# Optimization experiments

Measured on AMD Instinct MI355X. Metric: run time of the kernel, lower is better.

Reference implementation:

```python
import jax, jax.numpy as jnp
import numpy as np

B, L, D, H = 2, 2048, 1024, 16
DK = D // H


def setup_inputs() -> dict:
    key = jax.random.key(0)
    ks = jax.random.split(key, 12)
    s = 1.0 / np.sqrt(D)
    inp = {
        "query": jax.random.normal(ks[0], (B, L, D), jnp.float32),
        "key_": jax.random.normal(ks[1], (B, L, D), jnp.float32),
        "value": jax.random.normal(ks[2], (B, L, D), jnp.float32),
        # causal boolean mask, broadcast over heads: (B, 1, L_q, L_k)
        "mask": jnp.broadcast_to(jnp.tril(jnp.ones((L, L), jnp.bool_)), (B, 1, L, L)),
        "w_q": jax.random.uniform(ks[3], (D, D), jnp.float32, -s, s),
        "b_q": jax.random.uniform(ks[4], (D,), jnp.float32, -s, s),
        "w_k": jax.random.uniform(ks[5], (D, D), jnp.float32, -s, s),
        "b_k": jax.random.uniform(ks[6], (D,), jnp.float32, -s, s),
        "w_v": jax.random.uniform(ks[7], (D, D), jnp.float32, -s, s),
        "b_v": jax.random.uniform(ks[8], (D,), jnp.float32, -s, s),
        "w_o": jax.random.uniform(ks[9], (D, D), jnp.float32, -s, s),
        "b_o": jax.random.uniform(ks[10], (D,), jnp.float32, -s, s),
    }
    return inp


def reference(query, key_, value, mask, w_q, b_q, w_k, b_k, w_v, b_v, w_o, b_o):
    # torch nn.Linear: y = x @ W.T + b, weight shape (out, in)
    Q = query @ w_q.T + b_q
    K = key_ @ w_k.T + b_k
    V = value @ w_v.T + b_v
    # (B, L, H, DK) -> (B, H, L, DK)
    Q = Q.reshape(B, L, H, DK).transpose(0, 2, 1, 3)
    K = K.reshape(B, L, H, DK).transpose(0, 2, 1, 3)
    V = V.reshape(B, L, H, DK).transpose(0, 2, 1, 3)
    scaling = jnp.sqrt(jnp.float32(DK))
    scores = jnp.einsum("bhqd,bhkd->bhqk", Q, K) / scaling  # (B,H,L,L)
    scores = jnp.where(mask, scores, jnp.float32(-1e9))
    attn = jax.nn.softmax(scores, axis=-1)
    out = jnp.einsum("bhqk,bhkd->bhqd", attn, V)  # (B,H,L,DK)
    out = out.transpose(0, 2, 1, 3).reshape(B, L, D)
    return out @ w_o.T + b_o
```

## Files before the change

### kernel.cpp

```cpp
#include <hip/hip_runtime.h>
#include <stdint.h>

#define Bb 2
#define Ll 2048
#define Dd 1024
#define Hh 16
#define DKd 64
#define Mm (Bb*Ll)

typedef __bf16 bf16_t;
typedef __bf16 bf16x8 __attribute__((ext_vector_type(8)));
typedef float f32x4 __attribute__((ext_vector_type(4)));
typedef unsigned u32x2 __attribute__((ext_vector_type(2)));

#define AS1C(p) ((const __attribute__((address_space(1))) void*)(p))
#define AS3(p)  ((__attribute__((address_space(3))) void*)(p))

__device__ __forceinline__ unsigned short bfu(float f){
  return __builtin_bit_cast(unsigned short, (bf16_t)f);
}
__device__ __forceinline__ void wait_vm4(){ asm volatile("s_waitcnt vmcnt(4)" ::: "memory"); }
__device__ __forceinline__ void wait_vm6(){ asm volatile("s_waitcnt vmcnt(6)" ::: "memory"); }
__device__ __forceinline__ void wait_vm0(){ asm volatile("s_waitcnt vmcnt(0)" ::: "memory"); }
__device__ __forceinline__ void bar(){
  __builtin_amdgcn_sched_barrier(0);
  __builtin_amdgcn_s_barrier();
  __builtin_amdgcn_sched_barrier(0);
}

struct Cvt4 { const float* in[4]; ushort4* out[4]; };

__global__ void cvt_multi(Cvt4 a, int n4){
  const int z = blockIdx.y;
  int i = blockIdx.x*256 + threadIdx.x;
  if (i < n4){
    float4 v = ((const float4*)a.in[z])[i];
    ushort4 o; o.x=bfu(v.x); o.y=bfu(v.y); o.z=bfu(v.z); o.w=bfu(v.w);
    a.out[z][i] = o;
  }
}

struct GemmArgs {
  const void*   A[3];
  const bf16_t* W[3];
  const float*  bias[3];
  void*         out[3];
  float         scale[3];
  int           mode[3];
};

#define BKs 64

__global__ __launch_bounds__(256) void gemm128_f32(GemmArgs ga, int M, int N, int K)
{
  const int z = blockIdx.z;
  const float*  __restrict__ A  = (const float*)ga.A[z];
  const bf16_t* __restrict__ Bw = ga.W[z];
  const float*  __restrict__ bias = ga.bias[z];
  void* __restrict__ out = ga.out[z];
  const float scale = ga.scale[z];
  const int mode = ga.mode[z];

  __shared__ float  As[128*BKs];
  __shared__ bf16_t Bs[128*BKs];
  const int tid = threadIdx.x;
  const int lane = tid & 63;
  const int w = tid >> 6;
  const int m0 = blockIdx.x * 128;
  const int n0 = blockIdx.y * 128;
  const int wr = (w >> 1) * 64, wc = (w & 1) * 64;
  const int lrow16 = lane & 15;
  const int kgrp = lane >> 4;

  const int arow4 = lane >> 4;
  const int acb   = (lane & 15) * 16;
  const int brow8 = lane >> 3;
  const int bcb   = (lane & 7) * 16;

  f32x4 acc[4][4] = {};

  for (int k0 = 0; k0 < K; k0 += BKs) {
#pragma unroll
    for (int i = 0; i < 8; i++) {
      int c = i*4 + w;
      int row = c*4 + arow4;
      int sb = acb ^ ((row & 7) << 4);
      __builtin_amdgcn_global_load_lds(AS1C(A + (size_t)(m0+row)*K + k0 + (sb >> 2)),
                                       AS3((char*)As + c*1024), 16, 0, 0);
    }
#pragma unroll
    for (int i = 0; i < 4; i++) {
      int c = i*4 + w;
      int row = c*8 + brow8;
      int sb = bcb ^ ((row & 7) << 4);
      __builtin_amdgcn_global_load_lds(AS1C((const char*)(Bw + (size_t)(n0+row)*K + k0) + sb),
                                       AS3((char*)Bs + c*1024), 16, 0, 0);
    }
    __syncthreads();
#pragma unroll
    for (int ks = 0; ks < 2; ++ks) {
      bf16x8 af[4], bfr[4];
      const int akb = ks*128 + kgrp*32;
      const int bkb = ks*64 + kgrp*16;
#pragma unroll
      for (int m = 0; m < 4; m++) {
        int row = wr + m*16 + lrow16;
        int swz = (row & 7) << 4;
        const char* rb = (const char*)As + row*256;
        float4 lo = *(const float4*)(rb + (akb ^ swz));
        float4 hi = *(const float4*)(rb + ((akb + 16) ^ swz));
        bf16x8 a;
        a[0]=(bf16_t)lo.x; a[1]=(bf16_t)lo.y; a[2]=(bf16_t)lo.z; a[3]=(bf16_t)lo.w;
        a[4]=(bf16_t)hi.x; a[5]=(bf16_t)hi.y; a[6]=(bf16_t)hi.z; a[7]=(bf16_t)hi.w;
        af[m] = a;
      }
#pragma unroll
      for (int n = 0; n < 4; n++) {
        int row = wc + n*16 + lrow16;
        bfr[n] = *(const bf16x8*)((const char*)Bs + row*128 + (bkb ^ ((row & 7) << 4)));
      }
#pragma unroll
      for (int m = 0; m < 4; m++)
#pragma unroll
        for (int n = 0; n < 4; n++)
          acc[m][n] = __builtin_amdgcn_mfma_f32_16x16x32_bf16(af[m], bfr[n], acc[m][n], 0, 0, 0);
    }
    __syncthreads();
  }

#pragma unroll
  for (int m = 0; m < 4; m++)
#pragma unroll
    for (int n = 0; n < 4; n++) {
      const int row0 = m0 + wr + m*16 + kgrp*4;
      const int col  = n0 + wc + n*16 + lrow16;
      const float bcol = bias[col];
      if (mode == 2) {
        int b = row0 >> 11, l0 = row0 & 2047;
        int h = col >> 6, dk = col & 63;
        ushort4 u;
        u.x = bfu((acc[m][n][0] + bcol) * scale);
        u.y = bfu((acc[m][n][1] + bcol) * scale);
        u.z = bfu((acc[m][n][2] + bcol) * scale);
        u.w = bfu((acc[m][n][3] + bcol) * scale);
        *(ushort4*)((unsigned short*)out + ((size_t)((b<<4) + h)*DKd + dk)*Ll + l0) = u;
      } else {
#pragma unroll
        for (int i = 0; i < 4; i++) {
          int row = row0 + i;
          float v = (acc[m][n][i] + bcol) * scale;
          if (mode == 1) {
            ((float*)out)[(size_t)row*N + col] = v;
          } else {
            int b = row >> 11, l = row & 2047;
            int h = col >> 6, dk = col & 63;
            ((unsigned short*)out)[((size_t)((b<<4) + h)*Ll + l)*DKd + dk] = bfu(v);
          }
        }
      }
    }
}

#define BM 128
#define BN 64

__device__ __forceinline__ void stage_tile(
    const bf16_t* __restrict__ A, const bf16_t* __restrict__ Bw,
    int m0, int n0, int K, int k0, bf16_t* As, bf16_t* Bs,
    int w, int srow, int scol)
{
#pragma unroll
  for (int i = 0; i < 4; i++) {
    int c = i*4 + w;
    int row = c*8 + srow;
    int sc = scol ^ ((row & 7) << 3);
    __builtin_amdgcn_global_load_lds(AS1C(A + (size_t)(m0+row)*K + k0 + sc),
                                     AS3(As + c*512), 16, 0, 0);
  }
#pragma unroll
  for (int i = 0; i < 2; i++) {
    int c = i*4 + w;
    int row = c*8 + srow;
    int sc = scol ^ ((row & 7) << 3);
    __builtin_amdgcn_global_load_lds(AS1C(Bw + (size_t)(n0+row)*K + k0 + sc),
                                     AS3(Bs + c*512), 16, 0, 0);
  }
}

__global__ __launch_bounds__(256) void gemm_bt(GemmArgs ga, int M, int N, int K)
{
  const int z = blockIdx.z;
  const bf16_t* __restrict__ A  = (const bf16_t*)ga.A[z];
  const bf16_t* __restrict__ Bw = ga.W[z];
  const float*  __restrict__ bias = ga.bias[z];
  void* __restrict__ out = ga.out[z];
  const float scale = ga.scale[z];
  const int mode = ga.mode[z];

  __shared__ bf16_t As[2][BM*BKs];
  __shared__ bf16_t Bs[2][BN*BKs];
  const int tid = threadIdx.x;
  const int lane = tid & 63;
  const int w = tid >> 6;
  const int m0 = blockIdx.x * BM;
  const int n0 = blockIdx.y * BN;
  const int wr = (w >> 1) * 64, wc = (w & 1) * 32;
  const int lrow16 = lane & 15;
  const int kgrp = lane >> 4;
  const int srow = lane >> 3;
  const int scol = (lane & 7) * 8;

  f32x4 acc[4][2] = {};

  stage_tile(A, Bw, m0, n0, K, 0, As[0], Bs[0], w, srow, scol);

  const int KT = K / BKs;
  int cur = 0;
  for (int kt = 0; kt < KT; ++kt) {
    if (kt + 1 < KT) {
      stage_tile(A, Bw, m0, n0, K, (kt+1)*BKs, As[cur^1], Bs[cur^1], w, srow, scol);
      wait_vm6();
    } else {
      wait_vm0();
    }
    bar();
#pragma unroll
    for (int ks = 0; ks < 2; ++ks) {
      const int kbyte = ks*64 + kgrp*16;
      bf16x8 af[4], bfr[2];
#pragma unroll
      for (int m = 0; m < 4; m++) {
        int row = wr + m*16 + lrow16;
        af[m] = *(const bf16x8*)((const char*)As[cur] + row*128 + (kbyte ^ ((row & 7) << 4)));
      }
#pragma unroll
      for (int n = 0; n < 2; n++) {
        int row = wc + n*16 + lrow16;
        bfr[n] = *(const bf16x8*)((const char*)Bs[cur] + row*128 + (kbyte ^ ((row & 7) << 4)));
      }
#pragma unroll
      for (int m = 0; m < 4; m++)
#pragma unroll
        for (int n = 0; n < 2; n++)
          acc[m][n] = __builtin_amdgcn_mfma_f32_16x16x32_bf16(af[m], bfr[n], acc[m][n], 0, 0, 0);
    }
    bar();
    cur ^= 1;
  }

#pragma unroll
  for (int m = 0; m < 4; m++)
#pragma unroll
    for (int n = 0; n < 2; n++) {
      const int row0 = m0 + wr + m*16 + kgrp*4;
      const int col  = n0 + wc + n*16 + lrow16;
      const float bcol = bias[col];
      if (mode == 2) {
        int b = row0 >> 11, l0 = row0 & 2047;
        int h = col >> 6, dk = col & 63;
        ushort4 u;
        u.x = bfu((acc[m][n][0] + bcol) * scale);
        u.y = bfu((acc[m][n][1] + bcol) * scale);
        u.z = bfu((acc[m][n][2] + bcol) * scale);
        u.w = bfu((acc[m][n][3] + bcol) * scale);
        *(ushort4*)((unsigned short*)out + ((size_t)((b<<4) + h)*DKd + dk)*Ll + l0) = u;
      } else {
#pragma unroll
        for (int i = 0; i < 4; i++) {
          int row = row0 + i;
          float v = (acc[m][n][i] + bcol) * scale;
          if (mode == 1) {
            ((float*)out)[(size_t)row*N + col] = v;
          } else {
            int b = row >> 11, l = row & 2047;
            int h = col >> 6, dk = col & 63;
            ((unsigned short*)out)[((size_t)((b<<4) + h)*Ll + l)*DKd + dk] = bfu(v);
          }
        }
      }
    }
}

#define KVB 64

__global__ __launch_bounds__(256) void attn_kernel(
    const bf16_t* __restrict__ Qh, const bf16_t* __restrict__ Kh,
    const bf16_t* __restrict__ VTg, unsigned short* __restrict__ Oa)
{
  const int id = blockIdx.x;
  const int x = id & 7;
  const int rest = id >> 3;
  const int hq = rest >> 4;
  const int j  = rest & 15;
  const int bh = x + 8*hq;
  const int sA = j;
  const int qtB = 31 - j;

  const int tid = threadIdx.x, lane = tid & 63, w = tid >> 6;
  const int r = lane & 15, g = lane >> 4;

  const bf16_t* Qp  = Qh  + (size_t)bh * Ll * DKd;
  const bf16_t* Kp  = Kh  + (size_t)bh * Ll * DKd;
  const bf16_t* VTp = VTg + (size_t)bh * Ll * DKd;

  __shared__ bf16_t Klds[2][64*64];
  __shared__ bf16_t Vlds[2][64*64];
  __shared__ bf16_t Plds[4][16*64];

  int q0 = j * 64;
  bf16x8 qf[2], qB[2];
#pragma unroll
  for (int ks = 0; ks < 2; ++ks) {
    qf[ks] = *(const bf16x8*)(Qp + (size_t)(q0 + w*16 + r)*DKd + ks*32 + g*8);
    qB[ks] = *(const bf16x8*)(Qp + (size_t)(qtB*64 + w*16 + r)*DKd + ks*32 + g*8);
  }

  bf16x8 ones;
#pragma unroll
  for (int jj = 0; jj < 8; ++jj) ones[jj] = (bf16_t)1.0f;

  f32x4 accO[4] = {};
  f32x4 accL = {};
  float mrow = -1e30f;

  const int krow_l = lane >> 3;
  const int kcol_l = ((lane & 7)*16) ^ (krow_l << 4);
  char* Pw = (char*)&Plds[w][0];
  const int rsw = (r & 7) << 4;
  const int b_ = bh >> 4, h_ = bh & 15;

  auto pre_tiles = [&](int kv, int buf){
#pragma unroll
    for (int i = 0; i < 2; ++i) {
      int c = i*4 + w;
      __builtin_amdgcn_global_load_lds(
        AS1C((const char*)Kp + (size_t)(kv*KVB + c*8 + krow_l)*128 + kcol_l),
        AS3((char*)&Klds[buf][0] + c*1024), 16, 0, 0);
      __builtin_amdgcn_global_load_lds(
        AS1C((const char*)VTp + (size_t)(c*8 + krow_l)*4096 + kv*128 + kcol_l),
        AS3((char*)&Vlds[buf][0] + c*1024), 16, 0, 0);
    }
  };

  pre_tiles(0, 0);

  int cur = 0;
  for (int s = 0; s < 33; ++s) {
    if (s < 32) {
      int kv2 = (s < sA) ? s + 1 : s - sA;
      pre_tiles(kv2, cur^1);
      wait_vm4();
    } else {
      wait_vm0();
    }
    bar();

    const int kv0 = ((s <= sA) ? s : s - sA - 1) * KVB;

    const char* Kbase = (const char*)&Klds[cur][0];
    f32x4 sv[4] = {};
    __builtin_amdgcn_s_setprio(1);
#pragma unroll
    for (int ks = 0; ks < 2; ++ks) {
      const int kbyte = ks*64 + g*16;
#pragma unroll
      for (int n = 0; n < 4; ++n) {
        int row = n*16 + r;
        bf16x8 kf = *(const bf16x8*)(Kbase + row*128 + (kbyte ^ ((row & 7) << 4)));
        sv[n] = __builtin_amdgcn_mfma_f32_16x16x32_bf16(kf, qf[ks], sv[n], 0, 0, 0);
      }
    }
    __builtin_amdgcn_s_setprio(0);

    if (s == sA || s == 32) {
      const int qg = q0 + w*16 + r;
#pragma unroll
      for (int n = 0; n < 4; ++n)
#pragma unroll
        for (int i = 0; i < 4; ++i)
          if (kv0 + n*16 + g*4 + i > qg) sv[n][i] = -1e30f;
    }

    float m0 = fmaxf(fmaxf(sv[0][0], sv[0][1]), sv[0][2]);
    float m1 = fmaxf(fmaxf(sv[0][3], sv[1][0]), sv[1][1]);
    float m2 = fmaxf(fmaxf(sv[1][2], sv[1][3]), sv[2][0]);
    float m3 = fmaxf(fmaxf(sv[2][1], sv[2][2]), sv[2][3]);
    float m4 = fmaxf(fmaxf(sv[3][0], sv[3][1]), sv[3][2]);
    float mx = fmaxf(fmaxf(fmaxf(m0, m1), m2), fmaxf(fmaxf(m3, m4), sv[3][3]));
    if (__any(mx > mrow + 8.f)) {
      mx = fmaxf(mx, __shfl_xor(mx, 16));
      mx = fmaxf(mx, __shfl_xor(mx, 32));
      float mnew = fmaxf(mrow, mx);
      float corr = __builtin_amdgcn_exp2f(mrow - mnew);
      float c0 = __shfl(corr, g*4 + 0);
      float c1 = __shfl(corr, g*4 + 1);
      float c2 = __shfl(corr, g*4 + 2);
      float c3 = __shfl(corr, g*4 + 3);
#pragma unroll
      for (int n = 0; n < 4; ++n) {
        accO[n][0] *= c0; accO[n][1] *= c1; accO[n][2] *= c2; accO[n][3] *= c3;
      }
      accL[0] *= c0; accL[1] *= c1; accL[2] *= c2; accL[3] *= c3;
      mrow = mnew;
    }
#pragma unroll
    for (int n = 0; n < 4; ++n)
#pragma unroll
      for (int i = 0; i < 4; ++i)
        sv[n][i] = __builtin_amdgcn_exp2f(sv[n][i] - mrow);

#pragma unroll
    for (int n = 0; n < 4; ++n) {
      unsigned lo = (unsigned)bfu(sv[n][0]) | ((unsigned)bfu(sv[n][1]) << 16);
      unsigned hi = (unsigned)bfu(sv[n][2]) | ((unsigned)bfu(sv[n][3]) << 16);
      u32x2 pk; pk[0] = lo; pk[1] = hi;
      *(u32x2*)(Pw + r*128 + ((n*32 + g*8) ^ rsw)) = pk;
    }

    const char* Vbase = (const char*)&Vlds[cur][0];
    __builtin_amdgcn_s_setprio(1);
#pragma unroll
    for (int ks = 0; ks < 2; ++ks) {
      const int kbyte = ks*64 + g*16;
      bf16x8 pa = *(const bf16x8*)(Pw + r*128 + (kbyte ^ rsw));
      accL = __builtin_amdgcn_mfma_f32_16x16x32_bf16(pa, ones, accL, 0, 0, 0);
#pragma unroll
      for (int n = 0; n < 4; ++n) {
        int row = n*16 + r;
        bf16x8 vf = *(const bf16x8*)(Vbase + row*128 + (kbyte ^ ((row & 7) << 4)));
        accO[n] = __builtin_amdgcn_mfma_f32_16x16x32_bf16(pa, vf, accO[n], 0, 0, 0);
      }
    }
    __builtin_amdgcn_s_setprio(0);

    if (s == sA) {
#pragma unroll
      for (int i = 0; i < 4; ++i) {
        float inv = 1.f / accL[i];
        int q = q0 + w*16 + g*4 + i;
#pragma unroll
        for (int n = 0; n < 4; ++n)
          Oa[((size_t)(b_*Ll + q))*Dd + h_*DKd + n*16 + r] = bfu(accO[n][i] * inv);
      }
      q0 = qtB * 64;
      qf[0] = qB[0]; qf[1] = qB[1];
#pragma unroll
      for (int n = 0; n < 4; ++n) accO[n] = f32x4{};
      accL = f32x4{};
      mrow = -1e30f;
    }

    bar();
    cur ^= 1;
  }

#pragma unroll
  for (int i = 0; i < 4; ++i) {
    float inv = 1.f / accL[i];
    int q = q0 + w*16 + g*4 + i;
#pragma unroll
    for (int n = 0; n < 4; ++n)
      Oa[((size_t)(b_*Ll + q))*Dd + h_*DKd + n*16 + r] = bfu(accO[n][i] * inv);
  }
}

extern "C" void kernel_launch(void* const* d_in, const int* in_sizes, int n_in,
                              void* d_out, int out_size, void* d_ws, size_t ws_size,
                              hipStream_t stream)
{
  const float* q  = (const float*)d_in[0];
  const float* k  = (const float*)d_in[1];
  const float* v  = (const float*)d_in[2];
  const float* wq = (const float*)d_in[4];
  const float* bq = (const float*)d_in[5];
  const float* wk = (const float*)d_in[6];
  const float* bk = (const float*)d_in[7];
  const float* wv = (const float*)d_in[8];
  const float* bv = (const float*)d_in[9];
  const float* wo = (const float*)d_in[10];
  const float* bo = (const float*)d_in[11];

  char* ws = (char*)d_ws;
  bf16_t* Wq = (bf16_t*)(ws + 25165824);
  bf16_t* Wk = (bf16_t*)(ws + 27262976);
  bf16_t* Wv = (bf16_t*)(ws + 29360128);
  bf16_t* Wo = (bf16_t*)(ws + 31457280);
  bf16_t* Qh = (bf16_t*)(ws + 33554432);
  bf16_t* Kh = (bf16_t*)(ws + 41943040);
  bf16_t* VT = (bf16_t*)(ws + 50331648);
  bf16_t* Oa = (bf16_t*)(ws + 58720256);

  const int NW4 = Dd * Dd / 4;

  Cvt4 cv;
  cv.in[0]=wq; cv.out[0]=(ushort4*)Wq;
  cv.in[1]=wk; cv.out[1]=(ushort4*)Wk;
  cv.in[2]=wv; cv.out[2]=(ushort4*)Wv;
  cv.in[3]=wo; cv.out[3]=(ushort4*)Wo;
  cvt_multi<<<dim3(NW4/256, 4), 256, 0, stream>>>(cv, NW4);

  const float qscale = 0.125f * 1.4426950408889634f;
  GemmArgs gqkv;
  gqkv.A[0]=q; gqkv.A[1]=k; gqkv.A[2]=v;
  gqkv.W[0]=Wq; gqkv.W[1]=Wk; gqkv.W[2]=Wv;
  gqkv.bias[0]=bq; gqkv.bias[1]=bk; gqkv.bias[2]=bv;
  gqkv.out[0]=Qh; gqkv.out[1]=Kh; gqkv.out[2]=VT;
  gqkv.scale[0]=qscale; gqkv.scale[1]=1.0f; gqkv.scale[2]=1.0f;
  gqkv.mode[0]=0; gqkv.mode[1]=0; gqkv.mode[2]=2;
  gemm128_f32<<<dim3(Mm/128, Dd/128, 3), 256, 0, stream>>>(gqkv, Mm, Dd, Dd);

  attn_kernel<<<dim3(512), 256, 0, stream>>>(Qh, Kh, VT, (unsigned short*)Oa);

  GemmArgs go;
  go.A[0]=Oa; go.A[1]=Oa; go.A[2]=Oa;
  go.W[0]=Wo; go.W[1]=Wo; go.W[2]=Wo;
  go.bias[0]=bo; go.bias[1]=bo; go.bias[2]=bo;
  go.out[0]=d_out; go.out[1]=d_out; go.out[2]=d_out;
  go.scale[0]=1.0f; go.scale[1]=1.0f; go.scale[2]=1.0f;
  go.mode[0]=1; go.mode[1]=1; go.mode[2]=1;
  gemm_bt<<<dim3(Mm/BM, Dd/BN, 1), 256, 0, stream>>>(go, Mm, Dd, Dd);
}
```

Baseline: 109.6 us.

## Prefetch fp32 A into registers and double-buffer B in QKV projection GEMM

The QKV projection GEMM now loads the fp32 activation tile into registers for the next k-step while the current one computes, converts it to bf16 once, and stores it to LDS as bf16. The weight tile is double-buffered in LDS through async global-to-LDS loads. This is meant to overlap global-memory latency with MFMA work and to halve A's LDS footprint and read traffic by converting once instead of once per wave. The cost is more registers for the prefetched A, an extra barrier per iteration, and a single A buffer that is written only after the barrier.

```diff
diff --git a/kernel.cpp b/kernel.cpp
--- a/kernel.cpp
+++ b/kernel.cpp
@@ -22,6 +22,7 @@
 __device__ __forceinline__ void wait_vm4(){ asm volatile("s_waitcnt vmcnt(4)" ::: "memory"); }
 __device__ __forceinline__ void wait_vm6(){ asm volatile("s_waitcnt vmcnt(6)" ::: "memory"); }
 __device__ __forceinline__ void wait_vm0(){ asm volatile("s_waitcnt vmcnt(0)" ::: "memory"); }
+__device__ __forceinline__ void wait_lgkm0(){ asm volatile("s_waitcnt lgkmcnt(0)" ::: "memory"); }
 __device__ __forceinline__ void bar(){
   __builtin_amdgcn_sched_barrier(0);
   __builtin_amdgcn_s_barrier();
@@ -51,7 +52,7 @@
 
 #define BKs 64
 
-__global__ __launch_bounds__(256) void gemm128_f32(GemmArgs ga, int M, int N, int K)
+__global__ __launch_bounds__(256) void gemm128_ra(GemmArgs ga, int M, int N, int K)
 {
   const int z = blockIdx.z;
   const float*  __restrict__ A  = (const float*)ga.A[z];
@@ -61,8 +62,8 @@
   const float scale = ga.scale[z];
   const int mode = ga.mode[z];
 
-  __shared__ float  As[128*BKs];
-  __shared__ bf16_t Bs[128*BKs];
+  __shared__ bf16_t As[128*BKs];
+  __shared__ bf16_t Bs[2][128*BKs];
   const int tid = threadIdx.x;
   const int lane = tid & 63;
   const int w = tid >> 6;
@@ -72,52 +73,73 @@
   const int lrow16 = lane & 15;
   const int kgrp = lane >> 4;
 
-  const int arow4 = lane >> 4;
-  const int acb   = (lane & 15) * 16;
   const int brow8 = lane >> 3;
   const int bcb   = (lane & 7) * 16;
-
-  f32x4 acc[4][4] = {};
-
-  for (int k0 = 0; k0 < K; k0 += BKs) {
-#pragma unroll
-    for (int i = 0; i < 8; i++) {
-      int c = i*4 + w;
-      int row = c*4 + arow4;
-      int sb = acb ^ ((row & 7) << 4);
-      __builtin_amdgcn_global_load_lds(AS1C(A + (size_t)(m0+row)*K + k0 + (sb >> 2)),
-                                       AS3((char*)As + c*1024), 16, 0, 0);
-    }
-#pragma unroll
-    for (int i = 0; i < 4; i++) {
+  const int arow  = tid >> 3;
+  const int awb   = ((tid & 7) * 16) ^ ((arow & 7) << 4);
+
+  f32x4 ar[4][2];
+
+  auto loadA = [&](int k0){
+#pragma unroll
+    for (int i = 0; i < 4; ++i) {
+      const float* p = A + (size_t)(m0 + i*32 + arow)*K + k0 + (tid & 7)*8;
+      ar[i][0] = *(const f32x4*)p;
+      ar[i][1] = *(const f32x4*)(p + 4);
+    }
+  };
+  auto writeA = [&](){
+#pragma unroll
+    for (int i = 0; i < 4; ++i) {
+      bf16x8 a;
+      a[0]=(bf16_t)ar[i][0][0]; a[1]=(bf16_t)ar[i][0][1];
+      a[2]=(bf16_t)ar[i][0][2]; a[3]=(bf16_t)ar[i][0][3];
+      a[4]=(bf16_t)ar[i][1][0]; a[5]=(bf16_t)ar[i][1][1];
+      a[6]=(bf16_t)ar[i][1][2]; a[7]=(bf16_t)ar[i][1][3];
+      *(bf16x8*)((char*)As + (i*32 + arow)*128 + awb) = a;
+    }
+  };
+  auto stageB = [&](int k0, int buf){
+#pragma unroll
+    for (int i = 0; i < 4; ++i) {
       int c = i*4 + w;
       int row = c*8 + brow8;
       int sb = bcb ^ ((row & 7) << 4);
       __builtin_amdgcn_global_load_lds(AS1C((const char*)(Bw + (size_t)(n0+row)*K + k0) + sb),
-                                       AS3((char*)Bs + c*1024), 16, 0, 0);
-    }
-    __syncthreads();
+                                       AS3((char*)&Bs[buf][0] + c*1024), 16, 0, 0);
+    }
+  };
+
+  f32x4 acc[4][4] = {};
+
+  loadA(0);
+  stageB(0, 0);
+  wait_vm0();
+  writeA();
+  wait_lgkm0();
+  bar();
+
+  const int KT = K / BKs;
+  int cur = 0;
+  for (int kt = 0; kt < KT; ++kt) {
+    const bool pre = (kt + 1 < KT);
+    if (pre) {
+      loadA((kt+1)*BKs);
+      stageB((kt+1)*BKs, cur^1);
+    }
 #pragma unroll
     for (int ks = 0; ks < 2; ++ks) {
+      const int kbyte = ks*64 + kgrp*16;
       bf16x8 af[4], bfr[4];
-      const int akb = ks*128 + kgrp*32;
-      const int bkb = ks*64 + kgrp*16;
 #pragma unroll
       for (int m = 0; m < 4; m++) {
         int row = wr + m*16 + lrow16;
-        int swz = (row & 7) << 4;
-        const char* rb = (const char*)As + row*256;
-        float4 lo = *(const float4*)(rb + (akb ^ swz));
-        float4 hi = *(const float4*)(rb + ((akb + 16) ^ swz));
-        bf16x8 a;
-        a[0]=(bf16_t)lo.x; a[1]=(bf16_t)lo.y; a[2]=(bf16_t)lo.z; a[3]=(bf16_t)lo.w;
-        a[4]=(bf16_t)hi.x; a[5]=(bf16_t)hi.y; a[6]=(bf16_t)hi.z; a[7]=(bf16_t)hi.w;
-        af[m] = a;
+        af[m] = *(const bf16x8*)((const char*)As + row*128 + (kbyte ^ ((row & 7) << 4)));
       }
 #pragma unroll
       for (int n = 0; n < 4; n++) {
         int row = wc + n*16 + lrow16;
-        bfr[n] = *(const bf16x8*)((const char*)Bs + row*128 + (bkb ^ ((row & 7) << 4)));
+        bfr[n] = *(const bf16x8*)((const char*)&Bs[cur][0] + row*128 + (kbyte ^ ((row & 7) << 4)));
       }
 #pragma unroll
       for (int m = 0; m < 4; m++)
@@ -125,7 +147,15 @@
         for (int n = 0; n < 4; n++)
           acc[m][n] = __builtin_amdgcn_mfma_f32_16x16x32_bf16(af[m], bfr[n], acc[m][n], 0, 0, 0);
     }
-    __syncthreads();
+    if (pre) wait_vm4();
+    bar();
+    if (pre) {
+      writeA();
+      wait_vm0();
+      wait_lgkm0();
+    }
+    bar();
+    cur ^= 1;
   }
 
 #pragma unroll
@@ -507,7 +537,7 @@
   gqkv.out[0]=Qh; gqkv.out[1]=Kh; gqkv.out[2]=VT;
   gqkv.scale[0]=qscale; gqkv.scale[1]=1.0f; gqkv.scale[2]=1.0f;
   gqkv.mode[0]=0; gqkv.mode[1]=0; gqkv.mode[2]=2;
-  gemm128_f32<<<dim3(Mm/128, Dd/128, 3), 256, 0, stream>>>(gqkv, Mm, Dd, Dd);
+  gemm128_ra<<<dim3(Mm/128, Dd/128, 3), 256, 0, stream>>>(gqkv, Mm, Dd, Dd);
 
   attn_kernel<<<dim3(512), 256, 0, stream>>>(Qh, Kh, VT, (unsigned short*)Oa);
 
```

Measured after the change: 107.8 us. About the same (-1.6%).
